# Optimization experiments

Hardware: AMD Instinct MI355X
Metric: run time of the kernel (lower is better)

## Reference

```python
import jax, jax.numpy as jnp
import numpy as np
from jax import lax

D_MODEL = 768
D_STATE = 64
BATCH = 2
SEQ = 2048


def setup_inputs() -> dict:
    key = jax.random.key(0)
    ks = jax.random.split(key, 12)
    d, n = D_MODEL, D_STATE
    x = jax.random.normal(ks[0], (BATCH, SEQ, d), dtype=jnp.float32)
    ln_gamma = jnp.ones((d,), jnp.float32)
    ln_beta = jnp.zeros((d,), jnp.float32)
    # nn.Linear default init ~ U(-1/sqrt(d), 1/sqrt(d))
    s = 1.0 / np.sqrt(d)
    W_in = jax.random.uniform(ks[1], (d, d), jnp.float32, -s, s)
    b_in = jax.random.uniform(ks[2], (d,), jnp.float32, -s, s)
    log_A = jax.random.normal(ks[3], (d, n), jnp.float32)
    B_p = jax.random.normal(ks[4], (d, n), jnp.float32) * 0.1
    C_p = jax.random.normal(ks[5], (d, n), jnp.float32) * 0.1
    D_p = jnp.ones((d,), jnp.float32)
    log_dt = jax.random.uniform(ks[6], (d,), jnp.float32) * 0.01 - 2.0
    W_out = jax.random.uniform(ks[7], (d, d), jnp.float32, -s, s)
    b_out = jax.random.uniform(ks[8], (d,), jnp.float32, -s, s)
    return {
        "x": x, "ln_gamma": ln_gamma, "ln_beta": ln_beta,
        "W_in": W_in, "b_in": b_in, "log_A": log_A,
        "B_p": B_p, "C_p": C_p, "D_p": D_p, "log_dt": log_dt,
        "W_out": W_out, "b_out": b_out,
    }


def reference(x, ln_gamma, ln_beta, W_in, b_in, log_A, B_p, C_p, D_p, log_dt, W_out, b_out):
    residual = x
    # LayerNorm (eps=1e-5, elementwise affine)
    mu = jnp.mean(x, axis=-1, keepdims=True)
    var = jnp.var(x, axis=-1, keepdims=True)
    xn = (x - mu) / jnp.sqrt(var + 1e-5) * ln_gamma + ln_beta
    # in_proj (torch Linear: x @ W^T + b)
    u = xn @ W_in.T + b_in  # [B,S,d]
    # Discretization
    A = -jnp.exp(log_A)                     # [d,N]
    dt = jnp.exp(log_dt)[:, None]           # [d,1]
    A_bar = jnp.exp(dt * A)                 # [d,N]
    B_bar = B_p * dt                        # [d,N]
    b, s, d = u.shape
    h0 = jnp.zeros((b, d, D_STATE), u.dtype)
    u_t = jnp.transpose(u, (1, 0, 2))       # [S,B,d]

    def step(h, xt):
        # h: [B,d,N], xt: [B,d]
        h = A_bar * h + B_bar * xt[:, :, None]
        y = jnp.einsum('bdn,dn->bd', h, C_p) + D_p * xt
        return h, y

    _, ys = lax.scan(step, h0, u_t)         # ys: [S,B,d]
    y = jnp.transpose(ys, (1, 0, 2))        # [B,S,d]
    y = y @ W_out.T + b_out
    # dropout is identity in eval mode
    return y + residual
```

## Files before the change

### kernel.cpp

```cpp
#include <hip/hip_runtime.h>
#include <math.h>

#define D_MODEL 768
#define D_STATE 64
#define BATCH   2
#define SEQ     2048
#define M_TOTAL (BATCH * SEQ)

typedef unsigned short ushort_t;
typedef float f32x4 __attribute__((ext_vector_type(4)));
typedef __bf16 bf16x8 __attribute__((ext_vector_type(8)));

__device__ __forceinline__ ushort_t f2bf(float f) {
    unsigned u = __float_as_uint(f);
    u = (u + 0x7FFFu + ((u >> 16) & 1u)) >> 16;
    return (ushort_t)u;
}

__device__ __forceinline__ void gload16(const void* g, void* shm) {
    __builtin_amdgcn_global_load_lds(
        (const __attribute__((address_space(1))) void*)g,
        (__attribute__((address_space(3))) void*)shm, 16, 0, 0);
}

__global__ __launch_bounds__(256) void pre_kernel(const float* __restrict__ x,
                                                  const float* __restrict__ gamma,
                                                  const float* __restrict__ beta,
                                                  ushort_t* __restrict__ xnb,
                                                  const float* __restrict__ W_in,
                                                  const float* __restrict__ W_out,
                                                  ushort_t* __restrict__ Winb,
                                                  ushort_t* __restrict__ Woutb) {
    int bx = blockIdx.x;
    if (bx >= 1024) {
        int b2 = bx - 1024;
        const float* src = (b2 < 576) ? W_in : W_out;
        ushort_t*    dst = (b2 < 576) ? Winb : Woutb;
        int blk = (b2 < 576) ? b2 : b2 - 576;
        int i = (blk * 256 + threadIdx.x) * 4;
        float4 v = *(const float4*)(src + i);
        ushort4 o = make_ushort4(f2bf(v.x), f2bf(v.y), f2bf(v.z), f2bf(v.w));
        *(ushort4*)(dst + i) = o;
        return;
    }
    int row  = bx * 4 + (threadIdx.x >> 6);
    int lane = threadIdx.x & 63;
    const float* xr = x + (size_t)row * D_MODEL;
    float4 v[3];
    v[0] = *(const float4*)(xr + lane * 4);
    v[1] = *(const float4*)(xr + 256 + lane * 4);
    v[2] = *(const float4*)(xr + 512 + lane * 4);
    float s = 0.f, ss = 0.f;
#pragma unroll
    for (int i = 0; i < 3; ++i) {
        s  += v[i].x + v[i].y + v[i].z + v[i].w;
        ss += v[i].x * v[i].x + v[i].y * v[i].y + v[i].z * v[i].z + v[i].w * v[i].w;
    }
#pragma unroll
    for (int off = 1; off < 64; off <<= 1) {
        s  += __shfl_xor(s, off, 64);
        ss += __shfl_xor(ss, off, 64);
    }
    float mean = s * (1.0f / 768.0f);
    float var  = ss * (1.0f / 768.0f) - mean * mean;
    float inv  = 1.0f / sqrtf(var + 1e-5f);
    ushort_t* xo = xnb + (size_t)row * D_MODEL;
#pragma unroll
    for (int i = 0; i < 3; ++i) {
        int c = i * 256 + lane * 4;
        float4 g  = *(const float4*)(gamma + c);
        float4 bb = *(const float4*)(beta + c);
        ushort4 o = make_ushort4(f2bf((v[i].x - mean) * inv * g.x + bb.x),
                                 f2bf((v[i].y - mean) * inv * g.y + bb.y),
                                 f2bf((v[i].z - mean) * inv * g.z + bb.z),
                                 f2bf((v[i].w - mean) * inv * g.w + bb.w));
        *(ushort4*)(xo + c) = o;
    }
}


__global__ __launch_bounds__(256) void gemm_in(const ushort_t* __restrict__ A,
                                               const ushort_t* __restrict__ B,
                                               const float* __restrict__ bias,
                                               ushort_t* __restrict__ uTb) {
    __shared__ __align__(16) char smem[32768];
    float* T = (float*)smem;

    int tid = threadIdx.x;
    int w = tid >> 6, l = tid & 63;
    int bm = blockIdx.x * 64, bn = blockIdx.y * 64;
    int mq = (w & 1) * 32, nq = (w >> 1) * 32;

    int rowq = l >> 4;
    int segq = l & 15;

    float biasv[2];
#pragma unroll
    for (int nt = 0; nt < 2; ++nt)
        biasv[nt] = bias[bn + nq + nt * 16 + (l & 15)];

    f32x4 acc[2][2] = {};
    for (int k0 = 0; k0 < D_MODEL; k0 += 128) {
#pragma unroll
        for (int q = 0; q < 4; ++q) {
            int row = w * 16 + q * 4 + rowq;
            int col = k0 + ((segq ^ (row & 7)) * 8);
            gload16(A + (size_t)(bm + row) * D_MODEL + col, smem + w * 4096 + q * 1024);
            gload16(B + (size_t)(bn + row) * D_MODEL + col, smem + 16384 + w * 4096 + q * 1024);
        }
        __syncthreads();
#pragma unroll
        for (int kk = 0; kk < 4; ++kk) {
            int sgb = kk * 4 + (l >> 4);
            bf16x8 af[2], bf[2];
#pragma unroll
            for (int mt = 0; mt < 2; ++mt) {
                int r = mq + mt * 16 + (l & 15);
                af[mt] = *(const bf16x8*)(smem + r * 256 + ((sgb ^ (r & 7)) * 16));
            }
#pragma unroll
            for (int nt = 0; nt < 2; ++nt) {
                int r = nq + nt * 16 + (l & 15);
                bf[nt] = *(const bf16x8*)(smem + 16384 + r * 256 + ((sgb ^ (r & 7)) * 16));
            }
#pragma unroll
            for (int mt = 0; mt < 2; ++mt)
#pragma unroll
                for (int nt = 0; nt < 2; ++nt)
                    acc[mt][nt] = __builtin_amdgcn_mfma_f32_16x16x32_bf16(af[mt], bf[nt], acc[mt][nt], 0, 0, 0);
        }
        __syncthreads();
    }
#pragma unroll
    for (int mt = 0; mt < 2; ++mt)
#pragma unroll
        for (int nt = 0; nt < 2; ++nt)
#pragma unroll
            for (int i = 0; i < 4; ++i) {
                int nl = nq + nt * 16 + (l & 15);
                int ml = mq + mt * 16 + (l >> 4) * 4 + i;
                T[nl * 68 + ml] = acc[mt][nt][i] + biasv[nt];
            }
    __syncthreads();
    int b = bm >> 11, sbase = bm & 2047;
    int n = tid >> 2, mseg = (tid & 3) * 16;
    ushort_t* dst = uTb + ((size_t)b * D_MODEL + bn + n) * SEQ + sbase + mseg;
#pragma unroll
    for (int q = 0; q < 4; ++q) {
        float4 v = *(const float4*)&T[n * 68 + mseg + q * 4];
        ushort4 o = make_ushort4(f2bf(v.x), f2bf(v.y), f2bf(v.z), f2bf(v.w));
        *(ushort4*)(dst + q * 4) = o;
    }
}

__global__ __launch_bounds__(256) void gemm_out(const ushort_t* __restrict__ A,
                                                const ushort_t* __restrict__ B,
                                                const float* __restrict__ bias,
                                                const float* __restrict__ resid,
                                                float* __restrict__ out) {
    __shared__ __align__(16) char smem[32768];
    int tid = threadIdx.x;
    int w = tid >> 6, l = tid & 63;
    int bm = blockIdx.x * 64, bn = blockIdx.y * 64;
    int mq = (w & 1) * 32, nq = (w >> 1) * 32;

    int rowq = l >> 4;
    int segq = l & 15;

    float biasv[2];
#pragma unroll
    for (int nt = 0; nt < 2; ++nt)
        biasv[nt] = bias[bn + nq + nt * 16 + (l & 15)];

    f32x4 acc[2][2] = {};
    for (int k0 = 0; k0 < D_MODEL; k0 += 128) {
#pragma unroll
        for (int q = 0; q < 4; ++q) {
            int row = w * 16 + q * 4 + rowq;
            int col = k0 + ((segq ^ (row & 7)) * 8);
            gload16(A + (size_t)(bm + row) * D_MODEL + col, smem + w * 4096 + q * 1024);
            gload16(B + (size_t)(bn + row) * D_MODEL + col, smem + 16384 + w * 4096 + q * 1024);
        }
        __syncthreads();
#pragma unroll
        for (int kk = 0; kk < 4; ++kk) {
            int sgb = kk * 4 + (l >> 4);
            bf16x8 af[2], bf[2];
#pragma unroll
            for (int mt = 0; mt < 2; ++mt) {
                int r = mq + mt * 16 + (l & 15);
                af[mt] = *(const bf16x8*)(smem + r * 256 + ((sgb ^ (r & 7)) * 16));
            }
#pragma unroll
            for (int nt = 0; nt < 2; ++nt) {
                int r = nq + nt * 16 + (l & 15);
                bf[nt] = *(const bf16x8*)(smem + 16384 + r * 256 + ((sgb ^ (r & 7)) * 16));
            }
#pragma unroll
            for (int mt = 0; mt < 2; ++mt)
#pragma unroll
                for (int nt = 0; nt < 2; ++nt)
                    acc[mt][nt] = __builtin_amdgcn_mfma_f32_16x16x32_bf16(af[mt], bf[nt], acc[mt][nt], 0, 0, 0);
        }
        __syncthreads();
    }
#pragma unroll
    for (int mt = 0; mt < 2; ++mt)
#pragma unroll
        for (int i = 0; i < 4; ++i) {
            int m = bm + mq + mt * 16 + (l >> 4) * 4 + i;
            const float* rp = resid + (size_t)m * D_MODEL + bn;
            float* op = out + (size_t)m * D_MODEL + bn;
#pragma unroll
            for (int nt = 0; nt < 2; ++nt) {
                int nl = nq + nt * 16 + (l & 15);
                op[nl] = acc[mt][nt][i] + biasv[nt] + rp[nl];
            }
        }
}

#define OFF_U  0
#define OFF_V  9216
#define OFF_T  18432
#define OFF_M  27648
#define OFF_H  36864
#define OFF_W  46080
#define OFF_SM 63488

__global__ __launch_bounds__(256) void scan_mm(const ushort_t* __restrict__ uTb,
                                               const float* __restrict__ log_A,
                                               const float* __restrict__ B_p,
                                               const float* __restrict__ C_p,
                                               const float* __restrict__ D_p,
                                               const float* __restrict__ log_dt,
                                               float* __restrict__ yT) {
    __shared__ __align__(16) char smem[65024];
    ushort_t* Up = (ushort_t*)(smem + OFF_U);
    ushort_t* Vp = (ushort_t*)(smem + OFF_V);
    ushort_t* Tp = (ushort_t*)(smem + OFF_T);
    ushort_t* Mp = (ushort_t*)(smem + OFF_M);
    ushort_t* Hp = (ushort_t*)(smem + OFF_H);
    float*    Wp = (float*)(smem + OFF_W);
    float*    Kp = (float*)(smem + OFF_W);
    float*    aArr  = (float*)(smem + OFF_SM);
    float*    BbArr = aArr + 64;
    float*    CcArr = aArr + 128;
    float*    CBArr = aArr + 192;
    float*    Kc    = aArr + 256;

    int d   = blockIdx.x;
    int tid = threadIdx.x;
    int w   = tid >> 6, l = tid & 63;

    if (tid < 64) {
        int n = tid;
        float dt = __expf(log_dt[d]);
        float a  = -dt * __expf(log_A[d * 64 + n]);
        float Bb = B_p[d * 64 + n] * dt;
        float Cc = C_p[d * 64 + n];
        aArr[n] = a; BbArr[n] = Bb; CcArr[n] = Cc; CBArr[n] = Cc * Bb;
    }
    __syncthreads();

    {
        int tau = tid & 63, part = tid >> 6;
        float s = 0.f;
#pragma unroll
        for (int i = 0; i < 16; ++i) {
            int n = part * 16 + i;
            s += CBArr[n] * __expf((float)tau * aArr[n]);
        }
        Kp[part * 64 + tau] = s;
    }
    __syncthreads();
    if (tid < 64)
        Kc[tid] = Kp[tid] + Kp[64 + tid] + Kp[128 + tid] + Kp[192 + tid]
                + (tid == 0 ? D_p[d] : 0.f);
    __syncthreads();

    {
        int r = tid >> 2, seg = (tid & 3) * 16;
        float a = aArr[r], Bb = BbArr[r];
#pragma unroll
        for (int i = 0; i < 16; ++i) {
            int s = seg + i;
            Vp[r * 72 + s] = f2bf(Bb * __expf((float)(63 - s) * a));
        }
#pragma unroll
        for (int i = 0; i < 16; ++i) {
            int n = seg + i;
            Mp[r * 72 + n] = f2bf(CcArr[n] * __expf((float)(r + 1) * aArr[n]));
        }
#pragma unroll
        for (int i = 0; i < 16; ++i) {
            int s = seg + i;
            Tp[r * 72 + s] = (s <= r) ? f2bf(Kc[r - s]) : (ushort_t)0;
        }
        int col = r, bu = col >> 5, cu = col & 31;
        const ushort_t* usrc = uTb + ((size_t)bu * D_MODEL + d) * SEQ + cu * 64 + seg;
        *(uint4*)(Up + col * 72 + seg)     = *(const uint4*)(usrc);
        *(uint4*)(Up + col * 72 + seg + 8) = *(const uint4*)(usrc + 8);
    }
    __syncthreads();

    {
        int p0 = w * 16;
        f32x4 acc1[4] = {};
#pragma unroll
        for (int kk = 0; kk < 2; ++kk) {
            int koff = kk * 32 + (l >> 4) * 8;
            bf16x8 af = *(const bf16x8*)(Vp + (p0 + (l & 15)) * 72 + koff);
#pragma unroll
            for (int qt = 0; qt < 4; ++qt) {
                bf16x8 bf = *(const bf16x8*)(Up + (qt * 16 + (l & 15)) * 72 + koff);
                acc1[qt] = __builtin_amdgcn_mfma_f32_16x16x32_bf16(af, bf, acc1[qt], 0, 0, 0);
            }
        }
#pragma unroll
        for (int qt = 0; qt < 4; ++qt)
#pragma unroll
            for (int i = 0; i < 4; ++i)
                Wp[(qt * 16 + (l & 15)) * 68 + p0 + (l >> 4) * 4 + i] = acc1[qt][i];
    }
    __syncthreads();

    if (tid < 128) {
        int b2 = tid >> 6, n = tid & 63;
        float Ab64 = __expf(64.f * aArr[n]);
        float H = 0.f;
#pragma unroll
        for (int c = 0; c < 32; ++c) {
            int col = b2 * 32 + c;
            Hp[col * 72 + n] = f2bf(H);
            H = fmaf(Ab64, H, Wp[col * 68 + n]);
        }
    }
    __syncthreads();

    {
        int j0 = w * 16;
        f32x4 accY[4] = {};
#pragma unroll
        for (int kk = 0; kk < 2; ++kk) {
            int koff = kk * 32 + (l >> 4) * 8;
            bf16x8 at = *(const bf16x8*)(Tp + (j0 + (l & 15)) * 72 + koff);
            bf16x8 am = *(const bf16x8*)(Mp + (j0 + (l & 15)) * 72 + koff);
#pragma unroll
            for (int qt = 0; qt < 4; ++qt) {
                bf16x8 bu = *(const bf16x8*)(Up + (qt * 16 + (l & 15)) * 72 + koff);
                bf16x8 bh = *(const bf16x8*)(Hp + (qt * 16 + (l & 15)) * 72 + koff);
                accY[qt] = __builtin_amdgcn_mfma_f32_16x16x32_bf16(at, bu, accY[qt], 0, 0, 0);
                accY[qt] = __builtin_amdgcn_mfma_f32_16x16x32_bf16(am, bh, accY[qt], 0, 0, 0);
            }
        }
#pragma unroll
        for (int qt = 0; qt < 4; ++qt)
#pragma unroll
            for (int i = 0; i < 4; ++i)
                Wp[(qt * 16 + (l & 15)) * 68 + j0 + (l >> 4) * 4 + i] = accY[qt][i];
    }
    __syncthreads();

    {
        int col = tid >> 2, jseg = (tid & 3) * 16;
        int b3 = col >> 5, c3 = col & 31;
        float* dst = yT + ((size_t)b3 * D_MODEL + d) * SEQ + c3 * 64 + jseg;
#pragma unroll
        for (int q = 0; q < 4; ++q)
            *(float4*)(dst + q * 4) = *(const float4*)(Wp + col * 68 + jseg + q * 4);
    }
}

__global__ __launch_bounds__(256) void tcast_kernel(const float* __restrict__ yT,
                                                    ushort_t* __restrict__ yA) {
    __shared__ float T2[64 * 68];
    int t = threadIdx.x;
    int s0 = blockIdx.x * 64, d0 = blockIdx.y * 64, b = blockIdx.z;
    int dl = t >> 2, sq = (t & 3) * 16;
    const float* src = yT + ((size_t)b * D_MODEL + d0 + dl) * SEQ + s0 + sq;
#pragma unroll
    for (int q = 0; q < 4; ++q) {
        float4 v = *(const float4*)(src + q * 4);
        T2[(sq + q * 4 + 0) * 68 + dl] = v.x;
        T2[(sq + q * 4 + 1) * 68 + dl] = v.y;
        T2[(sq + q * 4 + 2) * 68 + dl] = v.z;
        T2[(sq + q * 4 + 3) * 68 + dl] = v.w;
    }
    __syncthreads();
    int sl = t >> 2, dseg = (t & 3) * 16;
    ushort_t* dst = yA + ((size_t)(b * SEQ + s0 + sl)) * D_MODEL + d0 + dseg;
#pragma unroll
    for (int q = 0; q < 4; ++q) {
        float4 v = *(const float4*)&T2[sl * 68 + dseg + q * 4];
        ushort4 o = make_ushort4(f2bf(v.x), f2bf(v.y), f2bf(v.z), f2bf(v.w));
        *(ushort4*)(dst + q * 4) = o;
    }
}

extern "C" void kernel_launch(void* const* d_in, const int* in_sizes, int n_in,
                              void* d_out, int out_size, void* d_ws, size_t ws_size,
                              hipStream_t stream) {
    const float* x        = (const float*)d_in[0];
    const float* ln_gamma = (const float*)d_in[1];
    const float* ln_beta  = (const float*)d_in[2];
    const float* W_in     = (const float*)d_in[3];
    const float* b_in     = (const float*)d_in[4];
    const float* log_A    = (const float*)d_in[5];
    const float* B_p      = (const float*)d_in[6];
    const float* C_p      = (const float*)d_in[7];
    const float* D_p      = (const float*)d_in[8];
    const float* log_dt   = (const float*)d_in[9];
    const float* W_out    = (const float*)d_in[10];
    const float* b_out    = (const float*)d_in[11];
    float* out = (float*)d_out;

    char* ws = (char*)d_ws;
    ushort_t* uTb   = (ushort_t*)(ws + 0);
    float*    yT    = (float*)(ws + 6291456);
    ushort_t* xnb   = (ushort_t*)(ws + 18874368);
    ushort_t* yA    = xnb;
    ushort_t* Winb  = (ushort_t*)(ws + 25165824);
    ushort_t* Woutb = (ushort_t*)(ws + 26345472);

    pre_kernel<<<dim3(1024 + 1152), 256, 0, stream>>>(x, ln_gamma, ln_beta, xnb,
                                                      W_in, W_out, Winb, Woutb);
    gemm_in<<<dim3(M_TOTAL / 64, D_MODEL / 64), 256, 0, stream>>>(xnb, Winb, b_in, uTb);
    scan_mm<<<dim3(D_MODEL), 256, 0, stream>>>(uTb, log_A, B_p, C_p, D_p, log_dt, yT);
    tcast_kernel<<<dim3(SEQ / 64, D_MODEL / 64, BATCH), 256, 0, stream>>>(yT, yA);
    gemm_out<<<dim3(M_TOTAL / 64, D_MODEL / 64), 256, 0, stream>>>(yA, Woutb, b_out, x, out);
}
```

Baseline: 128.3 us.

## Enlarge GEMM tiles to 128x96 and store scan output as bf16

Both projection GEMMs move from 64x64 tiles with 4 MFMA per wave to 128x96 tiles with 12 MFMA per wave and a K step of 64. This raises register-level reuse and cuts the grid from 768 to 256 blocks. The gemm_in epilogue is redone as two swizzled half passes through LDS. Separately, the scan writes its transposed output as bf16 instead of fp32, which halves that intermediate's traffic and makes the transpose kernel a plain 16-bit copy. The tradeoffs are fewer blocks (256 on a many-CU GPU) and one extra bf16 rounding in the scan output, which the later GEMM would have applied anyway.

```diff
diff --git a/kernel.cpp b/kernel.cpp
--- a/kernel.cpp
+++ b/kernel.cpp
@@ -83,73 +83,89 @@
                                                const ushort_t* __restrict__ B,
                                                const float* __restrict__ bias,
                                                ushort_t* __restrict__ uTb) {
-    __shared__ __align__(16) char smem[32768];
+    __shared__ __align__(16) char smem[28672];
     float* T = (float*)smem;
 
     int tid = threadIdx.x;
     int w = tid >> 6, l = tid & 63;
-    int bm = blockIdx.x * 64, bn = blockIdx.y * 64;
-    int mq = (w & 1) * 32, nq = (w >> 1) * 32;
-
-    int rowq = l >> 4;
-    int segq = l & 15;
-
-    float biasv[2];
-#pragma unroll
-    for (int nt = 0; nt < 2; ++nt)
-        biasv[nt] = bias[bn + nq + nt * 16 + (l & 15)];
-
-    f32x4 acc[2][2] = {};
-    for (int k0 = 0; k0 < D_MODEL; k0 += 128) {
+    int bm = blockIdx.x * 128, bn = blockIdx.y * 96;
+    int wr = w >> 1, wc = w & 1;
+
+    float biasv[3];
+#pragma unroll
+    for (int nt = 0; nt < 3; ++nt)
+        biasv[nt] = bias[bn + wc * 48 + nt * 16 + (l & 15)];
+
+    int lr = l >> 3;
+    int scol0 = ((l & 7) ^ lr) * 8;
+
+    f32x4 acc[4][3] = {};
+    for (int k0 = 0; k0 < D_MODEL; k0 += 64) {
 #pragma unroll
         for (int q = 0; q < 4; ++q) {
-            int row = w * 16 + q * 4 + rowq;
-            int col = k0 + ((segq ^ (row & 7)) * 8);
-            gload16(A + (size_t)(bm + row) * D_MODEL + col, smem + w * 4096 + q * 1024);
-            gload16(B + (size_t)(bn + row) * D_MODEL + col, smem + 16384 + w * 4096 + q * 1024);
-        }
-        __syncthreads();
-#pragma unroll
-        for (int kk = 0; kk < 4; ++kk) {
-            int sgb = kk * 4 + (l >> 4);
-            bf16x8 af[2], bf[2];
-#pragma unroll
-            for (int mt = 0; mt < 2; ++mt) {
-                int r = mq + mt * 16 + (l & 15);
-                af[mt] = *(const bf16x8*)(smem + r * 256 + ((sgb ^ (r & 7)) * 16));
-            }
-#pragma unroll
-            for (int nt = 0; nt < 2; ++nt) {
-                int r = nq + nt * 16 + (l & 15);
-                bf[nt] = *(const bf16x8*)(smem + 16384 + r * 256 + ((sgb ^ (r & 7)) * 16));
-            }
-#pragma unroll
-            for (int mt = 0; mt < 2; ++mt)
-#pragma unroll
-                for (int nt = 0; nt < 2; ++nt)
+            int row = w * 32 + q * 8 + lr;
+            gload16(A + (size_t)(bm + row) * D_MODEL + k0 + scol0, smem + w * 4096 + q * 1024);
+        }
+#pragma unroll
+        for (int q = 0; q < 3; ++q) {
+            int row = w * 24 + q * 8 + lr;
+            gload16(B + (size_t)(bn + row) * D_MODEL + k0 + scol0, smem + 16384 + w * 3072 + q * 1024);
+        }
+        __syncthreads();
+#pragma unroll
+        for (int kk = 0; kk < 2; ++kk) {
+            int seg = kk * 4 + (l >> 4);
+            bf16x8 af[4], bf[3];
+#pragma unroll
+            for (int mt = 0; mt < 4; ++mt) {
+                int r = wr * 64 + mt * 16 + (l & 15);
+                af[mt] = *(const bf16x8*)(smem + r * 128 + ((seg ^ (r & 7)) * 16));
+            }
+#pragma unroll
+            for (int nt = 0; nt < 3; ++nt) {
+                int r = wc * 48 + nt * 16 + (l & 15);
+                bf[nt] = *(const bf16x8*)(smem + 16384 + r * 128 + ((seg ^ (r & 7)) * 16));
+            }
+#pragma unroll
+            for (int mt = 0; mt < 4; ++mt)
+#pragma unroll
+                for (int nt = 0; nt < 3; ++nt)
                     acc[mt][nt] = __builtin_amdgcn_mfma_f32_16x16x32_bf16(af[mt], bf[nt], acc[mt][nt], 0, 0, 0);
         }
         __syncthreads();
     }
-#pragma unroll
-    for (int mt = 0; mt < 2; ++mt)
-#pragma unroll
-        for (int nt = 0; nt < 2; ++nt)
-#pragma unroll
-            for (int i = 0; i < 4; ++i) {
-                int nl = nq + nt * 16 + (l & 15);
-                int ml = mq + mt * 16 + (l >> 4) * 4 + i;
-                T[nl * 68 + ml] = acc[mt][nt][i] + biasv[nt];
-            }
-    __syncthreads();
+
     int b = bm >> 11, sbase = bm & 2047;
-    int n = tid >> 2, mseg = (tid & 3) * 16;
-    ushort_t* dst = uTb + ((size_t)b * D_MODEL + bn + n) * SEQ + sbase + mseg;
-#pragma unroll
-    for (int q = 0; q < 4; ++q) {
-        float4 v = *(const float4*)&T[n * 68 + mseg + q * 4];
-        ushort4 o = make_ushort4(f2bf(v.x), f2bf(v.y), f2bf(v.z), f2bf(v.w));
-        *(ushort4*)(dst + q * 4) = o;
+#pragma unroll
+    for (int h = 0; h < 2; ++h) {
+        if (wc == h) {
+#pragma unroll
+            for (int nt = 0; nt < 3; ++nt) {
+                int n = nt * 16 + (l & 15);
+                float bv = biasv[nt];
+#pragma unroll
+                for (int mt = 0; mt < 4; ++mt) {
+                    int seg = wr * 16 + mt * 4 + (l >> 4);
+                    f32x4 v = acc[mt][nt];
+                    v.x += bv; v.y += bv; v.z += bv; v.w += bv;
+                    *(f32x4*)(T + n * 128 + ((seg ^ (n & 7)) * 4)) = v;
+                }
+            }
+        }
+        __syncthreads();
+        if (tid < 192) {
+            int n2 = tid >> 2;
+            int m0 = (tid & 3) * 32;
+            ushort_t* dst = uTb + ((size_t)b * D_MODEL + bn + h * 48 + n2) * SEQ + sbase + m0;
+#pragma unroll
+            for (int q = 0; q < 8; ++q) {
+                int seg = (m0 >> 2) + q;
+                f32x4 v = *(const f32x4*)(T + n2 * 128 + ((seg ^ (n2 & 7)) * 4));
+                ushort4 o = make_ushort4(f2bf(v.x), f2bf(v.y), f2bf(v.z), f2bf(v.w));
+                *(ushort4*)(dst + q * 4) = o;
+            }
+        }
+        __syncthreads();
     }
 }
 
@@ -158,62 +174,65 @@
                                                 const float* __restrict__ bias,
                                                 const float* __restrict__ resid,
                                                 float* __restrict__ out) {
-    __shared__ __align__(16) char smem[32768];
+    __shared__ __align__(16) char smem[28672];
     int tid = threadIdx.x;
     int w = tid >> 6, l = tid & 63;
-    int bm = blockIdx.x * 64, bn = blockIdx.y * 64;
-    int mq = (w & 1) * 32, nq = (w >> 1) * 32;
-
-    int rowq = l >> 4;
-    int segq = l & 15;
-
-    float biasv[2];
-#pragma unroll
-    for (int nt = 0; nt < 2; ++nt)
-        biasv[nt] = bias[bn + nq + nt * 16 + (l & 15)];
-
-    f32x4 acc[2][2] = {};
-    for (int k0 = 0; k0 < D_MODEL; k0 += 128) {
+    int bm = blockIdx.x * 128, bn = blockIdx.y * 96;
+    int wr = w >> 1, wc = w & 1;
+
+    float biasv[3];
+#pragma unroll
+    for (int nt = 0; nt < 3; ++nt)
+        biasv[nt] = bias[bn + wc * 48 + nt * 16 + (l & 15)];
+
+    int lr = l >> 3;
+    int scol0 = ((l & 7) ^ lr) * 8;
+
+    f32x4 acc[4][3] = {};
+    for (int k0 = 0; k0 < D_MODEL; k0 += 64) {
 #pragma unroll
         for (int q = 0; q < 4; ++q) {
-            int row = w * 16 + q * 4 + rowq;
-            int col = k0 + ((segq ^ (row & 7)) * 8);
-            gload16(A + (size_t)(bm + row) * D_MODEL + col, smem + w * 4096 + q * 1024);
-            gload16(B + (size_t)(bn + row) * D_MODEL + col, smem + 16384 + w * 4096 + q * 1024);
-        }
-        __syncthreads();
-#pragma unroll
-        for (int kk = 0; kk < 4; ++kk) {
-            int sgb = kk * 4 + (l >> 4);
-            bf16x8 af[2], bf[2];
-#pragma unroll
-            for (int mt = 0; mt < 2; ++mt) {
-                int r = mq + mt * 16 + (l & 15);
-                af[mt] = *(const bf16x8*)(smem + r * 256 + ((sgb ^ (r & 7)) * 16));
-            }
-#pragma unroll
-            for (int nt = 0; nt < 2; ++nt) {
-                int r = nq + nt * 16 + (l & 15);
-                bf[nt] = *(const bf16x8*)(smem + 16384 + r * 256 + ((sgb ^ (r & 7)) * 16));
-            }
-#pragma unroll
-            for (int mt = 0; mt < 2; ++mt)
-#pragma unroll
-                for (int nt = 0; nt < 2; ++nt)
+            int row = w * 32 + q * 8 + lr;
+            gload16(A + (size_t)(bm + row) * D_MODEL + k0 + scol0, smem + w * 4096 + q * 1024);
+        }
+#pragma unroll
+        for (int q = 0; q < 3; ++q) {
+            int row = w * 24 + q * 8 + lr;
+            gload16(B + (size_t)(bn + row) * D_MODEL + k0 + scol0, smem + 16384 + w * 3072 + q * 1024);
+        }
+        __syncthreads();
+#pragma unroll
+        for (int kk = 0; kk < 2; ++kk) {
+            int seg = kk * 4 + (l >> 4);
+            bf16x8 af[4], bf[3];
+#pragma unroll
+            for (int mt = 0; mt < 4; ++mt) {
+                int r = wr * 64 + mt * 16 + (l & 15);
+                af[mt] = *(const bf16x8*)(smem + r * 128 + ((seg ^ (r & 7)) * 16));
+            }
+#pragma unroll
+            for (int nt = 0; nt < 3; ++nt) {
+                int r = wc * 48 + nt * 16 + (l & 15);
+                bf[nt] = *(const bf16x8*)(smem + 16384 + r * 128 + ((seg ^ (r & 7)) * 16));
+            }
+#pragma unroll
+            for (int mt = 0; mt < 4; ++mt)
+#pragma unroll
+                for (int nt = 0; nt < 3; ++nt)
                     acc[mt][nt] = __builtin_amdgcn_mfma_f32_16x16x32_bf16(af[mt], bf[nt], acc[mt][nt], 0, 0, 0);
         }
         __syncthreads();
     }
 #pragma unroll
-    for (int mt = 0; mt < 2; ++mt)
+    for (int mt = 0; mt < 4; ++mt)
 #pragma unroll
         for (int i = 0; i < 4; ++i) {
-            int m = bm + mq + mt * 16 + (l >> 4) * 4 + i;
+            int m = bm + wr * 64 + mt * 16 + (l >> 4) * 4 + i;
             const float* rp = resid + (size_t)m * D_MODEL + bn;
             float* op = out + (size_t)m * D_MODEL + bn;
 #pragma unroll
-            for (int nt = 0; nt < 2; ++nt) {
-                int nl = nq + nt * 16 + (l & 15);
+            for (int nt = 0; nt < 3; ++nt) {
+                int nl = wc * 48 + nt * 16 + (l & 15);
                 op[nl] = acc[mt][nt][i] + biasv[nt] + rp[nl];
             }
         }
@@ -233,7 +252,7 @@
                                                const float* __restrict__ C_p,
                                                const float* __restrict__ D_p,
                                                const float* __restrict__ log_dt,
-                                               float* __restrict__ yT) {
+                                               ushort_t* __restrict__ yTb) {
     __shared__ __align__(16) char smem[65024];
     ushort_t* Up = (ushort_t*)(smem + OFF_U);
     ushort_t* Vp = (ushort_t*)(smem + OFF_V);
@@ -364,37 +383,36 @@
     {
         int col = tid >> 2, jseg = (tid & 3) * 16;
         int b3 = col >> 5, c3 = col & 31;
-        float* dst = yT + ((size_t)b3 * D_MODEL + d) * SEQ + c3 * 64 + jseg;
-#pragma unroll
-        for (int q = 0; q < 4; ++q)
-            *(float4*)(dst + q * 4) = *(const float4*)(Wp + col * 68 + jseg + q * 4);
-    }
-}
-
-__global__ __launch_bounds__(256) void tcast_kernel(const float* __restrict__ yT,
+        ushort_t* dst = yTb + ((size_t)b3 * D_MODEL + d) * SEQ + c3 * 64 + jseg;
+#pragma unroll
+        for (int q = 0; q < 4; ++q) {
+            f32x4 v = *(const f32x4*)(Wp + col * 68 + jseg + q * 4);
+            ushort4 o = make_ushort4(f2bf(v.x), f2bf(v.y), f2bf(v.z), f2bf(v.w));
+            *(ushort4*)(dst + q * 4) = o;
+        }
+    }
+}
+
+__global__ __launch_bounds__(256) void tcast_kernel(const ushort_t* __restrict__ yTb,
                                                     ushort_t* __restrict__ yA) {
-    __shared__ float T2[64 * 68];
+    __shared__ ushort_t T2[64 * 72];
     int t = threadIdx.x;
     int s0 = blockIdx.x * 64, d0 = blockIdx.y * 64, b = blockIdx.z;
     int dl = t >> 2, sq = (t & 3) * 16;
-    const float* src = yT + ((size_t)b * D_MODEL + d0 + dl) * SEQ + s0 + sq;
-#pragma unroll
-    for (int q = 0; q < 4; ++q) {
-        float4 v = *(const float4*)(src + q * 4);
-        T2[(sq + q * 4 + 0) * 68 + dl] = v.x;
-        T2[(sq + q * 4 + 1) * 68 + dl] = v.y;
-        T2[(sq + q * 4 + 2) * 68 + dl] = v.z;
-        T2[(sq + q * 4 + 3) * 68 + dl] = v.w;
-    }
+    const ushort_t* src = yTb + ((size_t)b * D_MODEL + d0 + dl) * SEQ + s0 + sq;
+    uint4 v01 = *(const uint4*)(src);
+    uint4 v23 = *(const uint4*)(src + 8);
+    const ushort_t* pv = (const ushort_t*)&v01;
+#pragma unroll
+    for (int j = 0; j < 8; ++j) T2[(sq + j) * 72 + dl] = pv[j];
+    pv = (const ushort_t*)&v23;
+#pragma unroll
+    for (int j = 0; j < 8; ++j) T2[(sq + 8 + j) * 72 + dl] = pv[j];
     __syncthreads();
     int sl = t >> 2, dseg = (t & 3) * 16;
     ushort_t* dst = yA + ((size_t)(b * SEQ + s0 + sl)) * D_MODEL + d0 + dseg;
-#pragma unroll
-    for (int q = 0; q < 4; ++q) {
-        float4 v = *(const float4*)&T2[sl * 68 + dseg + q * 4];
-        ushort4 o = make_ushort4(f2bf(v.x), f2bf(v.y), f2bf(v.z), f2bf(v.w));
-        *(ushort4*)(dst + q * 4) = o;
-    }
+    *(uint4*)(dst)     = *(const uint4*)&T2[sl * 72 + dseg];
+    *(uint4*)(dst + 8) = *(const uint4*)&T2[sl * 72 + dseg + 8];
 }
 
 extern "C" void kernel_launch(void* const* d_in, const int* in_sizes, int n_in,
@@ -416,16 +434,16 @@
 
     char* ws = (char*)d_ws;
     ushort_t* uTb   = (ushort_t*)(ws + 0);
-    float*    yT    = (float*)(ws + 6291456);
-    ushort_t* xnb   = (ushort_t*)(ws + 18874368);
+    ushort_t* yTb   = (ushort_t*)(ws + 6291456);
+    ushort_t* xnb   = (ushort_t*)(ws + 12582912);
     ushort_t* yA    = xnb;
-    ushort_t* Winb  = (ushort_t*)(ws + 25165824);
-    ushort_t* Woutb = (ushort_t*)(ws + 26345472);
+    ushort_t* Winb  = (ushort_t*)(ws + 18874368);
+    ushort_t* Woutb = (ushort_t*)(ws + 20054016);
 
     pre_kernel<<<dim3(1024 + 1152), 256, 0, stream>>>(x, ln_gamma, ln_beta, xnb,
                                                       W_in, W_out, Winb, Woutb);
-    gemm_in<<<dim3(M_TOTAL / 64, D_MODEL / 64), 256, 0, stream>>>(xnb, Winb, b_in, uTb);
-    scan_mm<<<dim3(D_MODEL), 256, 0, stream>>>(uTb, log_A, B_p, C_p, D_p, log_dt, yT);
-    tcast_kernel<<<dim3(SEQ / 64, D_MODEL / 64, BATCH), 256, 0, stream>>>(yT, yA);
-    gemm_out<<<dim3(M_TOTAL / 64, D_MODEL / 64), 256, 0, stream>>>(yA, Woutb, b_out, x, out);
-}
+    gemm_in<<<dim3(M_TOTAL / 128, D_MODEL / 96), 256, 0, stream>>>(xnb, Winb, b_in, uTb);
+    scan_mm<<<dim3(D_MODEL), 256, 0, stream>>>(uTb, log_A, B_p, C_p, D_p, log_dt, yTb);
+    tcast_kernel<<<dim3(SEQ / 64, D_MODEL / 64, BATCH), 256, 0, stream>>>(yTb, yA);
+    gemm_out<<<dim3(M_TOTAL / 128, D_MODEL / 96), 256, 0, stream>>>(yA, Woutb, b_out, x, out);
+}
```

Result: slower. 136.2 us (+6.2%).
